# Kernel tuning notes

Measured on AMD Instinct MI355X. Metric: run time of the kernel, lower is better.

The kernel has to match this reference:

```python
import jax, jax.numpy as jnp
import numpy as np

VOCAB = 100000
N_NODES = 200000
D = 128


def setup_inputs() -> dict:
    key = jax.random.key(0)
    k1, k2, k3, k4, k5, k6 = jax.random.split(key, 6)
    nodes = jax.random.randint(k1, (N_NODES,), 0, VOCAB, dtype=jnp.int64 if jax.config.jax_enable_x64 else jnp.int32).astype(jnp.int32)
    c2e_weight = jax.random.normal(k2, (VOCAB, D), dtype=jnp.float32)
    w1 = jax.random.normal(k3, (D, D), dtype=jnp.float32) * (1.0 / np.sqrt(D))
    b1 = jax.random.normal(k4, (D,), dtype=jnp.float32) * 0.01
    w2 = jax.random.normal(k5, (D, D), dtype=jnp.float32) * (1.0 / np.sqrt(D))
    b2 = jax.random.normal(k6, (D,), dtype=jnp.float32) * 0.01
    return {"nodes": nodes, "c2e_weight": c2e_weight, "w1": w1, "b1": b1, "w2": w2, "b2": b2}


def reference(nodes, c2e_weight, w1, b1, w2, b2):
    # Vectorized version of the per-node Python loop:
    #   ce = c2e.weight[node]; x = relu(w_r1(ce)); out = relu(w_r2(x))
    ce = c2e_weight[nodes]                         # [N, D] gather
    h = jax.nn.relu(ce @ w1.T + b1)                # [N, D]
    out = jax.nn.relu(h @ w2.T + b2)               # [N, D]
    return out
```

## Files before the change

### kernel.cpp

```cpp
#include <hip/hip_runtime.h>
#include <hip/hip_bf16.h>

#define D_DIM   128
#define MT      64
#define NBLOCKS 512
#define NTHR    512

typedef __attribute__((ext_vector_type(8))) short bf16x8;
typedef __attribute__((ext_vector_type(4))) float f32x4;

__device__ __forceinline__ unsigned short f2bf(float f) {
    return __builtin_bit_cast(unsigned short, __float2bfloat16(f));
}

__device__ __forceinline__ int sw_off(int row, int col) {
    return row * 128 + ((((col >> 3) ^ (row & 15)) << 3) | (col & 7));
}

__device__ __forceinline__ void stage_w(const float* __restrict__ w,
                                        unsigned short* __restrict__ sW, int t) {
    #pragma unroll
    for (int i = 0; i < 8; ++i) {
        const int idx4 = i * NTHR + t;
        const float4 v = ((const float4*)w)[idx4];
        const int row = idx4 >> 5;
        const int c4  = (idx4 & 31) * 4;
        ushort4 b;
        b.x = f2bf(v.x); b.y = f2bf(v.y); b.z = f2bf(v.z); b.w = f2bf(v.w);
        *(ushort4*)&sW[sw_off(row, c4)] = b;
    }
}

__global__ __launch_bounds__(NTHR, 2)
void ctx_encoder(const int* __restrict__ nodes,
                 const float* __restrict__ c2e,
                 const float* __restrict__ w1,
                 const float* __restrict__ b1,
                 const float* __restrict__ w2,
                 const float* __restrict__ b2,
                 float* __restrict__ out,
                 int N) {
    __shared__ unsigned short sW1[D_DIM * 128];
    __shared__ unsigned short sW2[D_DIM * 128];
    __shared__ unsigned short sX [MT    * 128];

    const int t    = threadIdx.x;
    const int lane = t & 63;
    const int wave = t >> 6;
    const int pair = wave >> 1;
    const int half = wave & 1;
    const int cl   = lane & 15;
    const int quad = lane >> 4;

    const int grow0 = t >> 3;
    const int gc    = t & 7;

    stage_w(w1, sW1, t);
    stage_w(w2, sW2, t);

    float bias1[4], bias2[4];
    #pragma unroll
    for (int c = 0; c < 4; ++c) {
        const int j = (half * 4 + c) * 16 + cl;
        bias1[c] = b1[j];
        bias2[c] = b2[j];
    }

    const int nTiles = (N + MT - 1) / MT;
    int tl = blockIdx.x;

    int r0 = tl * MT + grow0;  r0 = r0 < N ? r0 : N - 1;
    int idx_cur = nodes[r0];
    float4 g[4];
    {
        const float* rp = c2e + (size_t)idx_cur * D_DIM + gc * 4;
        #pragma unroll
        for (int i = 0; i < 4; ++i)
            g[i] = *(const float4*)(rp + i * 32);
    }
    int idx_nxt = 0;
    if (tl + NBLOCKS < nTiles) {
        int r1 = (tl + NBLOCKS) * MT + grow0;  r1 = r1 < N ? r1 : N - 1;
        idx_nxt = nodes[r1];
    }
    __syncthreads();

    while (tl < nTiles) {
        #pragma unroll
        for (int i = 0; i < 4; ++i) {
            ushort4 b;
            b.x = f2bf(g[i].x); b.y = f2bf(g[i].y);
            b.z = f2bf(g[i].z); b.w = f2bf(g[i].w);
            *(ushort4*)&sX[sw_off(grow0, gc * 4 + i * 32)] = b;
        }
        __syncthreads();

        bf16x8 aF[4];
        #pragma unroll
        for (int ks = 0; ks < 4; ++ks)
            aF[ks] = *(const bf16x8*)&sX[sw_off(pair * 16 + cl, ks * 32 + quad * 8)];

        const int tn = tl + NBLOCKS;
        if (tn < nTiles) {
            const float* rp = c2e + (size_t)idx_nxt * D_DIM + gc * 4;
            #pragma unroll
            for (int i = 0; i < 4; ++i)
                g[i] = *(const float4*)(rp + i * 32);
            if (tn + NBLOCKS < nTiles) {
                int rn = (tn + NBLOCKS) * MT + grow0;  rn = rn < N ? rn : N - 1;
                idx_nxt = nodes[rn];
            }
        }
        __syncthreads();

        #pragma unroll
        for (int c = 0; c < 4; ++c) {
            const int ct = half * 4 + c;
            bf16x8 bF[4];
            #pragma unroll
            for (int ks = 0; ks < 4; ++ks)
                bF[ks] = *(const bf16x8*)&sW1[sw_off(ct * 16 + cl, ks * 32 + quad * 8)];
            f32x4 acc = {0.f, 0.f, 0.f, 0.f};
            #pragma unroll
            for (int ks = 0; ks < 4; ++ks)
                acc = __builtin_amdgcn_mfma_f32_16x16x32_bf16(aF[ks], bF[ks], acc, 0, 0, 0);
            const int j = ct * 16 + cl;
            #pragma unroll
            for (int r = 0; r < 4; ++r) {
                float h = acc[r] + bias1[c];
                h = h > 0.f ? h : 0.f;
                sX[sw_off(pair * 16 + quad * 4 + r, j)] = f2bf(h);
            }
        }
        __syncthreads();

        bf16x8 hF[4];
        #pragma unroll
        for (int ks = 0; ks < 4; ++ks)
            hF[ks] = *(const bf16x8*)&sX[sw_off(pair * 16 + cl, ks * 32 + quad * 8)];
        __syncthreads();

        const size_t obase = (size_t)tl * MT;
        #pragma unroll
        for (int c = 0; c < 4; ++c) {
            const int ct = half * 4 + c;
            bf16x8 bF[4];
            #pragma unroll
            for (int ks = 0; ks < 4; ++ks)
                bF[ks] = *(const bf16x8*)&sW2[sw_off(ct * 16 + cl, ks * 32 + quad * 8)];
            f32x4 acc = {0.f, 0.f, 0.f, 0.f};
            #pragma unroll
            for (int ks = 0; ks < 4; ++ks)
                acc = __builtin_amdgcn_mfma_f32_16x16x32_bf16(hF[ks], bF[ks], acc, 0, 0, 0);
            const int j = ct * 16 + cl;
            #pragma unroll
            for (int r = 0; r < 4; ++r) {
                float o = acc[r] + bias2[c];
                o = o > 0.f ? o : 0.f;
                const long grow = (long)(obase + pair * 16 + quad * 4 + r);
                if (grow < N)
                    out[(size_t)grow * D_DIM + j] = o;
            }
        }

        tl += NBLOCKS;
    }
}

extern "C" void kernel_launch(void* const* d_in, const int* in_sizes, int n_in,
                              void* d_out, int out_size, void* d_ws, size_t ws_size,
                              hipStream_t stream) {
    const int*   nodes = (const int*)d_in[0];
    const float* c2e   = (const float*)d_in[1];
    const float* w1    = (const float*)d_in[2];
    const float* b1    = (const float*)d_in[3];
    const float* w2    = (const float*)d_in[4];
    const float* b2    = (const float*)d_in[5];
    float* out = (float*)d_out;
    const int N = in_sizes[0];

    ctx_encoder<<<dim3(NBLOCKS), dim3(NTHR), 0, stream>>>(nodes, c2e, w1, b1, w2, b2, out, N);
}
```

Baseline: 164.9 us.

## Deepen gather prefetch to two tiles ahead, use nontemporal output stores

The loop is restructured to handle two tiles per iteration with two register buffers, so the embedding-row gather runs two tiles ahead and node indices are loaded four tiles ahead. Index loads are clamped to the last tile, which removes the bounds branches. Output writes become nontemporal stores, and the launch bound rises to four blocks per CU. The goal is to hide more gather latency, but the extra live registers together with the tighter register cap may cause spills. LDS use (about 80KB per block) probably still limits the kernel to two resident blocks per CU.

```diff
diff --git a/kernel.cpp b/kernel.cpp
--- a/kernel.cpp
+++ b/kernel.cpp
@@ -31,7 +31,7 @@
     }
 }
 
-__global__ __launch_bounds__(NTHR, 2)
+__global__ __launch_bounds__(NTHR, 4)
 void ctx_encoder(const int* __restrict__ nodes,
                  const float* __restrict__ c2e,
                  const float* __restrict__ w1,
@@ -67,25 +67,34 @@
     }
 
     const int nTiles = (N + MT - 1) / MT;
-    int tl = blockIdx.x;
+    const int lastT  = nTiles - 1;
 
-    int r0 = tl * MT + grow0;  r0 = r0 < N ? r0 : N - 1;
-    int idx_cur = nodes[r0];
-    float4 g[4];
-    {
-        const float* rp = c2e + (size_t)idx_cur * D_DIM + gc * 4;
+    auto loadIdx = [&](int tt) -> int {
+        tt = tt < lastT ? tt : lastT;
+        int r = tt * MT + grow0;
+        r = r < N ? r : N - 1;
+        return nodes[r];
+    };
+    auto gather = [&](int idx, float4* g) {
+        const float* rp = c2e + (size_t)idx * D_DIM + gc * 4;
         #pragma unroll
         for (int i = 0; i < 4; ++i)
             g[i] = *(const float4*)(rp + i * 32);
-    }
-    int idx_nxt = 0;
-    if (tl + NBLOCKS < nTiles) {
-        int r1 = (tl + NBLOCKS) * MT + grow0;  r1 = r1 < N ? r1 : N - 1;
-        idx_nxt = nodes[r1];
-    }
+    };
+
+    int tl = blockIdx.x;
+    float4 g0[4], g1[4];
+
+    int idxA = loadIdx(tl);
+    gather(idxA, g0);
+    int idxB = loadIdx(tl + NBLOCKS);
+    gather(idxB, g1);
+    int idxN0 = loadIdx(tl + 2 * NBLOCKS);
+    int idxN1 = loadIdx(tl + 3 * NBLOCKS);
+
     __syncthreads();
 
-    while (tl < nTiles) {
+    auto body = [&](int tcur, float4* g, int& idxRef) {
         #pragma unroll
         for (int i = 0; i < 4; ++i) {
             ushort4 b;
@@ -100,17 +109,8 @@
         for (int ks = 0; ks < 4; ++ks)
             aF[ks] = *(const bf16x8*)&sX[sw_off(pair * 16 + cl, ks * 32 + quad * 8)];
 
-        const int tn = tl + NBLOCKS;
-        if (tn < nTiles) {
-            const float* rp = c2e + (size_t)idx_nxt * D_DIM + gc * 4;
-            #pragma unroll
-            for (int i = 0; i < 4; ++i)
-                g[i] = *(const float4*)(rp + i * 32);
-            if (tn + NBLOCKS < nTiles) {
-                int rn = (tn + NBLOCKS) * MT + grow0;  rn = rn < N ? rn : N - 1;
-                idx_nxt = nodes[rn];
-            }
-        }
+        gather(idxRef, g);
+        idxRef = loadIdx(tcur + 4 * NBLOCKS);
         __syncthreads();
 
         #pragma unroll
@@ -140,7 +140,7 @@
             hF[ks] = *(const bf16x8*)&sX[sw_off(pair * 16 + cl, ks * 32 + quad * 8)];
         __syncthreads();
 
-        const size_t obase = (size_t)tl * MT;
+        const size_t obase = (size_t)tcur * MT;
         #pragma unroll
         for (int c = 0; c < 4; ++c) {
             const int ct = half * 4 + c;
@@ -159,11 +159,15 @@
                 o = o > 0.f ? o : 0.f;
                 const long grow = (long)(obase + pair * 16 + quad * 4 + r);
                 if (grow < N)
-                    out[(size_t)grow * D_DIM + j] = o;
+                    __builtin_nontemporal_store(o, &out[(size_t)grow * D_DIM + j]);
             }
         }
+    };
 
-        tl += NBLOCKS;
+    for (; tl < nTiles; tl += 2 * NBLOCKS) {
+        body(tl, g0, idxN0);
+        if (tl + NBLOCKS < nTiles)
+            body(tl + NBLOCKS, g1, idxN1);
     }
 }
 
```

After: 217.9 us. 32.1% more time.
